# Performance work log

Hardware: AMD Instinct MI355X
Metric: run time of the kernel (lower is better)

Reference implementation:

```python
import jax, jax.numpy as jnp
from jax import lax
import numpy as np

D_IN, D, H, W, POOL = 1280, 100, 20, 3, 9
K_SIG, X0 = 1.0, 0.0
EPS = 1e-5


def setup_inputs() -> dict:
    key = jax.random.key(0)
    ks = jax.random.split(key, 8)
    N1, N2 = 512, 512
    return {
        "x1": jax.random.normal(ks[0], (N1, D_IN), jnp.float32),
        "x2": jax.random.normal(ks[1], (N2, D_IN), jnp.float32),
        "W1": jax.random.normal(ks[2], (D, D_IN), jnp.float32) * 0.02,
        "b1": jnp.zeros((D,), jnp.float32),
        "W2": jax.random.normal(ks[3], (H, 2 * D), jnp.float32) * 0.05,
        "b2": jnp.zeros((H,), jnp.float32),
        "bn1_g": jnp.ones((H,), jnp.float32),
        "bn1_b": jnp.zeros((H,), jnp.float32),
        "conv_w": jax.random.normal(ks[4], (1, H, 2 * W + 1, 2 * W + 1), jnp.float32) * 0.05,
        "conv_b": jnp.zeros((1,), jnp.float32),
        "bn2_g": jnp.ones((1,), jnp.float32),
        "bn2_b": jnp.zeros((1,), jnp.float32),
        "gamma": jnp.zeros((1,), jnp.float32),
    }


def reference(x1, x2, W1, b1, W2, b2, bn1_g, bn1_b, conv_w, conv_b, bn2_g, bn2_b, gamma):
    N1, N2 = x1.shape[0], x2.shape[0]
    # fc1 projection (relu1/dropout1 are defined but unused in the original forward)
    a = (x1 @ W1.T + b1)[None]          # [1, N1, D]
    c = (x2 @ W1.T + b2 * 0 + b1)[None] if False else (x2 @ W1.T + b1)[None]  # [1, N2, D]
    # broadcast pairwise |diff| and product -> [1, N1, N2, 2D]
    diff = jnp.abs(a[:, :, None, :] - c[:, None, :, :])
    mul = a[:, :, None, :] * c[:, None, :, :]
    m = jnp.concatenate([diff, mul], axis=-1).reshape(-1, 2 * D)  # [N1*N2, 2D]
    # fc2
    m = m @ W2.T + b2                    # [N1*N2, H]
    # BatchNorm1d in training mode: batch statistics, biased variance
    mu = m.mean(axis=0)
    var = m.var(axis=0)
    m = (m - mu) * lax.rsqrt(var + EPS) * bn1_g + bn1_b
    m = jax.nn.relu(m)
    m = m.reshape(1, N1, N2, H).transpose(0, 3, 1, 2)  # NCHW [1, H, N1, N2]
    # 7x7 conv, padding=W
    C = lax.conv_general_dilated(m, conv_w, (1, 1), [(W, W), (W, W)])
    C = C + conv_b.reshape(1, -1, 1, 1)
    # BatchNorm2d (training mode, biased variance over N,H,W per channel)
    mu2 = C.mean(axis=(0, 2, 3), keepdims=True)
    var2 = C.var(axis=(0, 2, 3), keepdims=True)
    C = (C - mu2) * lax.rsqrt(var2 + EPS) * bn2_g.reshape(1, -1, 1, 1) + bn2_b.reshape(1, -1, 1, 1)
    C = jax.nn.sigmoid(C)
    # MaxPool2d(9, padding=4): stride = kernel, -inf padding
    p = POOL // 2
    B = lax.reduce_window(C, -jnp.inf, lax.max, (1, 1, POOL, POOL), (1, 1, POOL, POOL),
                          [(0, 0), (0, 0), (p, p), (p, p)])
    # mean / unbiased std over dims (1, 2) keepdim
    mean = B.mean(axis=(1, 2), keepdims=True)
    std = jnp.sqrt(B.var(axis=(1, 2), keepdims=True, ddof=1) + EPS)
    Q = jax.nn.relu(B - mean - gamma.reshape(()) * std)
    phat = Q.sum() / (jnp.sign(Q).sum() + 1.0)
    phat = jnp.clip(jax.nn.sigmoid(K_SIG * (phat - X0)), 0.0, 1.0)
    return phat, C
```

## Files before the change

kernel.cpp:

```cpp
#include <hip/hip_runtime.h>
#include <hip/hip_bf16.h>
#include <math.h>

#define N1 512
#define N2 512
#define DIN 1280
#define DD 100
#define HH 20
#define NPIX (N1*N2)
#define PB 57

typedef short bf16x8 __attribute__((ext_vector_type(8)));
typedef float f32x4 __attribute__((ext_vector_type(4)));

static constexpr size_t WS_PP    = 0;
static constexpr size_t WS_W1T   = 409600;
static constexpr size_t WS_W2B   = 537600;
static constexpr size_t WS_M     = 541696;
static constexpr size_t WS_CRAW  = WS_M + 5242880;
static constexpr size_t WS_STATS = WS_CRAW + 262144;
static constexpr size_t WS_B     = WS_STATS + 64;

__global__ __launch_bounds__(256) void kP(const float* __restrict__ W1,
                                          const float* __restrict__ W2,
                                          float* __restrict__ w1t,
                                          unsigned short* __restrict__ w2b,
                                          float* __restrict__ stats) {
  const int tid = threadIdx.x;
  if (blockIdx.x >= 160) {
    int idx = (blockIdx.x - 160) * 256 + tid;
    if (blockIdx.x == 160 && tid < 64) stats[tid] = 0.0f;
    if (idx < 224 * 32) {
      int k = idx >> 5, n = idx & 31;
      float v = (n < HH && k < 200) ? W2[n * 200 + k] : 0.0f;
      __hip_bfloat16 b = __float2bfloat16(v);
      w2b[idx] = *reinterpret_cast<unsigned short*>(&b);
    }
    return;
  }
  __shared__ float sT[32][33];
  const int bx = blockIdx.x % 40, by = blockIdx.x / 40;
  const int tx = tid & 31, ty = tid >> 5;
#pragma unroll
  for (int e = 0; e < 4; ++e) {
    int h = by * 32 + ty + e * 8, k = bx * 32 + tx;
    sT[ty + e * 8][tx] = (h < DD) ? W1[(size_t)h * DIN + k] : 0.0f;
  }
  __syncthreads();
#pragma unroll
  for (int e = 0; e < 4; ++e) {
    int k = bx * 32 + ty + e * 8, h = by * 32 + tx;
    if (h < DD) w1t[(size_t)k * DD + h] = sT[tx][ty + e * 8];
  }
}

__global__ __launch_bounds__(256) void kA(const float* __restrict__ x1,
                                          const float* __restrict__ x2,
                                          const float* __restrict__ w1t,
                                          float* __restrict__ pp) {
  const int tid = threadIdx.x;
  const int w  = __builtin_amdgcn_readfirstlane(tid >> 6);
  const int rp = w >> 1, hh = w & 1;
  const int h = hh * 64 + (tid & 63);
  if (h >= DD) return;
  const int kq = blockIdx.x & 3;
  const int r0 = (blockIdx.x >> 2) * 4 + rp * 2;
  const float* xb = (r0 < N1) ? (x1 + (size_t)r0 * DIN) : (x2 + (size_t)(r0 - N1) * DIN);
  const float* xr0 = xb + kq * 320;
  const float* xr1 = xb + DIN + kq * 320;
  const float* w1p = w1t + (size_t)kq * 320 * DD + h;
  float a00 = 0.f, a01 = 0.f, a10 = 0.f, a11 = 0.f;
#pragma unroll 8
  for (int k = 0; k < 320; k += 2) {
    float wA = w1p[(size_t)k * DD];
    float wB = w1p[(size_t)(k + 1) * DD];
    a00 = fmaf(wA, xr0[k], a00); a01 = fmaf(wB, xr0[k + 1], a01);
    a10 = fmaf(wA, xr1[k], a10); a11 = fmaf(wB, xr1[k + 1], a11);
  }
  pp[(size_t)kq * 102400 + (size_t)r0 * DD + h] = a00 + a01;
  pp[(size_t)kq * 102400 + (size_t)(r0 + 1) * DD + h] = a10 + a11;
}

__global__ __launch_bounds__(256, 2) void kB(const float* __restrict__ pp,
                                             const float* __restrict__ b1,
                                             const unsigned short* __restrict__ w2b,
                                             float* __restrict__ m,
                                             float* __restrict__ stats) {
  __shared__ float sA[8][132];
  __shared__ float sC[64][132];
  __shared__ float wred[4][40];
  const int tid = threadIdx.x;
  const int bi = blockIdx.x >> 3, bj = blockIdx.x & 7;
  for (int idx = tid; idx < 72 * 33; idx += 256) {
    int r = idx / 33, d4 = idx % 33;
    float4 v = {0.f, 0.f, 0.f, 0.f};
    if (d4 < 25) {
      size_t row = (r < 8) ? (size_t)(bi * 8 + r) : (size_t)(N1 + bj * 64 + (r - 8));
      const float* base = pp + row * DD;
      float4 a0 = ((const float4*)base)[d4];
      float4 a1 = ((const float4*)(base + 102400))[d4];
      float4 a2 = ((const float4*)(base + 204800))[d4];
      float4 a3 = ((const float4*)(base + 307200))[d4];
      float4 bb = ((const float4*)b1)[d4];
      v.x = a0.x + a1.x + a2.x + a3.x + bb.x;
      v.y = a0.y + a1.y + a2.y + a3.y + bb.y;
      v.z = a0.z + a1.z + a2.z + a3.z + bb.z;
      v.w = a0.w + a1.w + a2.w + a3.w + bb.w;
    }
    if (r < 8) *(float4*)&sA[r][4 * d4] = v;
    else       *(float4*)&sC[r - 8][4 * d4] = v;
  }
  __syncthreads();
  const int w = tid >> 6, lane = tid & 63;
  const int ln = lane & 15, q = lane >> 4;
  const int jj = w * 16 + ln;
  bf16x8 af[7][2];
#pragma unroll
  for (int ks = 0; ks < 7; ++ks)
#pragma unroll
    for (int t = 0; t < 2; ++t) {
      bf16x8 v;
#pragma unroll
      for (int e = 0; e < 8; ++e)
        v[e] = (short)w2b[(ks * 32 + q * 8 + e) * 32 + ln + 16 * t];
      af[ks][t] = v;
    }
  int dOf[14];
  bool isP[14];
  float4 cH[14];
#pragma unroll
  for (int hx = 0; hx < 14; ++hx) {
    int kk = (hx >> 1) * 32 + q * 8 + (hx & 1) * 4;
    isP[hx] = kk >= 100;
    dOf[hx] = isP[hx] ? kk - 100 : kk;
    cH[hx] = *(const float4*)&sC[jj][dOf[hx]];
  }
  float st_s[8], st_q[8];
#pragma unroll
  for (int r = 0; r < 8; ++r) { st_s[r] = 0.f; st_q[r] = 0.f; }
  const int gj = bj * 64 + jj;
#pragma unroll 1
  for (int ii = 0; ii < 8; ++ii) {
    bf16x8 bf[7];
#pragma unroll
    for (int ks = 0; ks < 7; ++ks) {
      float4 a0 = *(const float4*)&sA[ii][dOf[2 * ks]];
      float4 a1 = *(const float4*)&sA[ii][dOf[2 * ks + 1]];
      float4 c0 = cH[2 * ks], c1 = cH[2 * ks + 1];
      float f0 = isP[2*ks]   ? a0.x * c0.x : fabsf(a0.x - c0.x);
      float f1 = isP[2*ks]   ? a0.y * c0.y : fabsf(a0.y - c0.y);
      float f2 = isP[2*ks]   ? a0.z * c0.z : fabsf(a0.z - c0.z);
      float f3 = isP[2*ks]   ? a0.w * c0.w : fabsf(a0.w - c0.w);
      float f4 = isP[2*ks+1] ? a1.x * c1.x : fabsf(a1.x - c1.x);
      float f5 = isP[2*ks+1] ? a1.y * c1.y : fabsf(a1.y - c1.y);
      float f6 = isP[2*ks+1] ? a1.z * c1.z : fabsf(a1.z - c1.z);
      float f7 = isP[2*ks+1] ? a1.w * c1.w : fabsf(a1.w - c1.w);
      union { bf16x8 v; __hip_bfloat162 h2[4]; } u;
      u.h2[0] = __float22bfloat162_rn(make_float2(f0, f1));
      u.h2[1] = __float22bfloat162_rn(make_float2(f2, f3));
      u.h2[2] = __float22bfloat162_rn(make_float2(f4, f5));
      u.h2[3] = __float22bfloat162_rn(make_float2(f6, f7));
      bf[ks] = u.v;
    }
    f32x4 acc0 = {0.f, 0.f, 0.f, 0.f}, acc1 = {0.f, 0.f, 0.f, 0.f};
#pragma unroll
    for (int ks = 0; ks < 7; ++ks) {
      acc0 = __builtin_amdgcn_mfma_f32_16x16x32_bf16(af[ks][0], bf[ks], acc0, 0, 0, 0);
      acc1 = __builtin_amdgcn_mfma_f32_16x16x32_bf16(af[ks][1], bf[ks], acc1, 0, 0, 0);
    }
    const size_t pix = (size_t)(bi * 8 + ii) * N2 + gj;
#pragma unroll
    for (int r = 0; r < 4; ++r) {
      m[(size_t)(4 * q + r) * NPIX + pix] = acc0[r];
      st_s[r] += acc0[r];
      st_q[r] += acc0[r] * acc0[r];
    }
    if (q == 0) {
#pragma unroll
      for (int r = 0; r < 4; ++r)
        m[(size_t)(16 + r) * NPIX + pix] = acc1[r];
    }
#pragma unroll
    for (int r = 0; r < 4; ++r) {
      st_s[4 + r] += acc1[r];
      st_q[4 + r] += acc1[r] * acc1[r];
    }
  }
#pragma unroll
  for (int r = 0; r < 8; ++r) {
#pragma unroll
    for (int off = 1; off < 16; off <<= 1) {
      st_s[r] += __shfl_xor(st_s[r], off);
      st_q[r] += __shfl_xor(st_q[r], off);
    }
  }
  if (ln == 0) {
#pragma unroll
    for (int r = 0; r < 4; ++r) {
      wred[w][4 * q + r]      = st_s[r];
      wred[w][20 + 4 * q + r] = st_q[r];
    }
    if (q == 0) {
#pragma unroll
      for (int r = 0; r < 4; ++r) {
        wred[w][16 + r] = st_s[4 + r];
        wred[w][36 + r] = st_q[4 + r];
      }
    }
  }
  __syncthreads();
  if (tid < 40)
    atomicAdd(&stats[tid], wred[0][tid] + wred[1][tid] + wred[2][tid] + wred[3][tid]);
}

__global__ __launch_bounds__(256, 2) void kD(const float* __restrict__ m,
                                             const float* __restrict__ bn1g,
                                             const float* __restrict__ bn1b,
                                             const float* __restrict__ cw,
                                             float* __restrict__ stats,
                                             float* __restrict__ Craw) {
  __shared__ float sIn[2][4][22][40];
  __shared__ float sSc[HH], sSh[HH];
  __shared__ float wsum[4][2];
  const int tid = threadIdx.x;
  if (tid < HH) {
    float s = stats[tid], q = stats[HH + tid];
    float mu = s * (1.0f / NPIX);
    float var = q * (1.0f / NPIX) - mu * mu;
    float g = bn1g[tid] / sqrtf(var + 1e-5f);
    sSc[tid] = g;
    sSh[tid] = bn1b[tid] - mu * g;
  }
  const int by = (blockIdx.x >> 4) * 16, bx = (blockIdx.x & 15) * 32;
  const int w = tid >> 6, lane = tid & 63;
  const int gxs = bx + lane - 4;
  const bool colOk = (lane < 40) && (gxs >= 0) && (gxs < N2);
  float ld[22];
  {
    const float* mp = m + (size_t)w * NPIX + gxs;
#pragma unroll
    for (int r = 0; r < 22; ++r) {
      int gy = by + r - 3;
      ld[r] = (colOk && gy >= 0 && gy < N1) ? mp[(size_t)gy * N2] : 0.0f;
    }
  }
  __syncthreads();
  if (lane < 40) {
    float sc = sSc[w], sh = sSh[w];
#pragma unroll
    for (int r = 0; r < 22; ++r) {
      int gy = by + r - 3;
      bool ok = colOk && gy >= 0 && gy < N1;
      sIn[0][w][r][lane] = ok ? fmaxf(fmaf(ld[r], sc, sh), 0.0f) : 0.0f;
    }
  }
  __syncthreads();
  const int ty = tid >> 4, tx = tid & 15;
  float acc00 = 0.f, acc01 = 0.f;
#pragma unroll 1
  for (int cc = 0; cc < 5; ++cc) {
    if (cc < 4) {
      const float* mp = m + (size_t)((cc + 1) * 4 + w) * NPIX + gxs;
#pragma unroll
      for (int r = 0; r < 22; ++r) {
        int gy = by + r - 3;
        ld[r] = (colOk && gy >= 0 && gy < N1) ? mp[(size_t)gy * N2] : 0.0f;
      }
    }
    const int cur = cc & 1;
#pragma unroll 1
    for (int ch4 = 0; ch4 < 4; ++ch4) {
      float2 win[7][5];
#pragma unroll
      for (int rr = 0; rr < 7; ++rr)
#pragma unroll
        for (int qq = 0; qq < 5; ++qq)
          win[rr][qq] = *(const float2*)&sIn[cur][ch4][ty + rr][2 * tx + 2 * qq];
      const float* wch = cw + (cc * 4 + ch4) * 49;
#pragma unroll
      for (int ky = 0; ky < 7; ++ky)
#pragma unroll
        for (int kx = 0; kx < 7; ++kx) {
          float wt = wch[ky * 7 + kx];
          float e0 = ((kx + 1) & 1) ? win[ky][(kx + 1) >> 1].y : win[ky][(kx + 1) >> 1].x;
          float e1 = ((kx + 2) & 1) ? win[ky][(kx + 2) >> 1].y : win[ky][(kx + 2) >> 1].x;
          acc00 = fmaf(e0, wt, acc00);
          acc01 = fmaf(e1, wt, acc01);
        }
    }
    __syncthreads();
    if (cc < 4 && lane < 40) {
      int ch = (cc + 1) * 4 + w;
      float sc = sSc[ch], sh = sSh[ch];
#pragma unroll
      for (int r = 0; r < 22; ++r) {
        int gy = by + r - 3;
        bool ok = colOk && gy >= 0 && gy < N1;
        sIn[cur ^ 1][w][r][lane] = ok ? fmaxf(fmaf(ld[r], sc, sh), 0.0f) : 0.0f;
      }
    }
    __syncthreads();
  }
  const int oy = by + ty, ox = bx + 2 * tx;
  float2 r0 = {acc00, acc01};
  *(float2*)&Craw[(size_t)oy * N2 + ox] = r0;
  float s = acc00 + acc01;
  float q = acc00 * acc00 + acc01 * acc01;
#pragma unroll
  for (int off = 32; off; off >>= 1) {
    s += __shfl_xor(s, off);
    q += __shfl_xor(q, off);
  }
  if (lane == 0) { wsum[w][0] = s; wsum[w][1] = q; }
  __syncthreads();
  if (tid < 2) {
    float v = wsum[0][tid] + wsum[1][tid] + wsum[2][tid] + wsum[3][tid];
    atomicAdd(&stats[2 * HH + tid], v);
  }
}

__global__ __launch_bounds__(256) void kE2M(const float* __restrict__ Craw,
                                            const float* __restrict__ stats,
                                            const float* __restrict__ bn2g,
                                            const float* __restrict__ bn2b,
                                            float* __restrict__ Cout,
                                            float* __restrict__ B) {
  const int w = blockIdx.x * 4 + (threadIdx.x >> 6);
  const int lane = threadIdx.x & 63;
  float s = stats[2 * HH], q = stats[2 * HH + 1];
  float mu = s * (1.0f / NPIX);
  float var = q * (1.0f / NPIX) - mu * mu;
  float g = bn2g[0] / sqrtf(var + 1e-5f);
  float b = bn2b[0] - mu * g;
  if (w >= PB * PB) return;
  const int wy = w / PB, wx = w % PB;
  const int y0 = wy * 9 - 4, x0 = wx * 9 - 4;
  float mx = -1e30f;
  for (int e = lane; e < 144; e += 64) {
    int dy = e / 12, dx = e % 12;
    int y = y0 + dy, x = x0 + dx;
    bool inWin = (dy < 9) && (dx < 9);
    bool claim = (y >= 0) && (y < N1) && (x >= 0) && (x < N2) &&
                 (dy < 9 || wy == PB - 1) && (dx < 9 || wx == PB - 1);
    if (claim) {
      float z = Craw[(size_t)y * N2 + x] * g + b;
      float sg = 1.0f / (1.0f + expf(-z));
      Cout[(size_t)y * N2 + x] = sg;
      if (inWin) mx = fmaxf(mx, sg);
    }
  }
#pragma unroll
  for (int off = 32; off; off >>= 1) mx = fmaxf(mx, __shfl_xor(mx, off));
  if (lane == 0) B[w] = mx;
}

__global__ __launch_bounds__(1024) void kF(const float* __restrict__ B,
                                           const float* __restrict__ gamma,
                                           float* __restrict__ out0) {
  __shared__ float sB[PB * PB];
  __shared__ float cm[PB], cs[PB];
  __shared__ float r1[16], r2[16];
  const int tid = threadIdx.x;
  for (int i = tid; i < PB * PB; i += 1024) sB[i] = B[i];
  __syncthreads();
  if (tid < PB * 16) {
    int c = tid >> 4, g = tid & 15;
    float s = 0.0f;
    for (int h = g; h < PB; h += 16) s += sB[h * PB + c];
#pragma unroll
    for (int off = 1; off < 16; off <<= 1) s += __shfl_xor(s, off);
    float mean = s / (float)PB;
    float v = 0.0f;
    for (int h = g; h < PB; h += 16) { float d = sB[h * PB + c] - mean; v += d * d; }
#pragma unroll
    for (int off = 1; off < 16; off <<= 1) v += __shfl_xor(v, off);
    if (g == 0) {
      cm[c] = mean;
      cs[c] = sqrtf(v / (float)(PB - 1) + 1e-5f);
    }
  }
  __syncthreads();
  const float g = gamma[0];
  float sq = 0.0f, cnt = 0.0f;
  for (int i = tid; i < PB * PB; i += 1024) {
    int w = i % PB;
    float qv = sB[i] - cm[w] - g * cs[w];
    if (qv > 0.0f) { sq += qv; cnt += 1.0f; }
  }
#pragma unroll
  for (int off = 32; off; off >>= 1) {
    sq += __shfl_xor(sq, off);
    cnt += __shfl_xor(cnt, off);
  }
  if ((tid & 63) == 0) { r1[tid >> 6] = sq; r2[tid >> 6] = cnt; }
  __syncthreads();
  if (tid == 0) {
    float S = 0.f, Cn = 0.f;
#pragma unroll
    for (int e = 0; e < 16; ++e) { S += r1[e]; Cn += r2[e]; }
    float phat = S / (Cn + 1.0f);
    float sig = 1.0f / (1.0f + expf(-phat));
    out0[0] = fminf(fmaxf(sig, 0.0f), 1.0f);
  }
}

extern "C" void kernel_launch(void* const* d_in, const int* in_sizes, int n_in,
                              void* d_out, int out_size, void* d_ws, size_t ws_size,
                              hipStream_t stream) {
  const float* x1    = (const float*)d_in[0];
  const float* x2    = (const float*)d_in[1];
  const float* W1    = (const float*)d_in[2];
  const float* b1    = (const float*)d_in[3];
  const float* W2    = (const float*)d_in[4];
  const float* bn1g  = (const float*)d_in[6];
  const float* bn1b  = (const float*)d_in[7];
  const float* convw = (const float*)d_in[8];
  const float* bn2g  = (const float*)d_in[10];
  const float* bn2b  = (const float*)d_in[11];
  const float* gamma = (const float*)d_in[12];

  float* ws    = (float*)d_ws;
  float* pp    = ws + WS_PP;
  float* w1t   = ws + WS_W1T;
  unsigned short* w2b = (unsigned short*)(ws + WS_W2B);
  float* m     = ws + WS_M;
  float* Craw  = ws + WS_CRAW;
  float* stats = ws + WS_STATS;
  float* Bp    = ws + WS_B;
  float* out   = (float*)d_out;

  kP<<<188, 256, 0, stream>>>(W1, W2, w1t, w2b, stats);
  kA<<<1024, 256, 0, stream>>>(x1, x2, w1t, pp);
  kB<<<512, 256, 0, stream>>>(pp, b1, w2b, m, stats);
  kD<<<512, 256, 0, stream>>>(m, bn1g, bn1b, convw, stats, Craw);
  kE2M<<<(PB * PB + 3) / 4, 256, 0, stream>>>(Craw, stats, bn2g, bn2b, out + 1, Bp);
  kF<<<1, 1024, 0, stream>>>(Bp, gamma, out);
}
```

Before: 92.17 us.

## Split conv over channel groups with register-blocked rows and separate reduction kernel

The 7x7 conv kernel is reworked so that each block handles one group of 4 input channels (grid y = 5) over a 32x32 tile. Each thread computes 4 output rows x 2 columns, which reuses every loaded shared-memory row across several outputs. Partial results for the 5 channel groups are written to a new workspace buffer. A new kernel kE1 then sums the partials, writes Craw and accumulates the BN2 statistics. The goal is more parallelism and less redundant LDS traffic, at the cost of an extra 5x NPIX partial write and read plus one more kernel launch.

```diff
diff --git a/kernel.cpp b/kernel.cpp
--- a/kernel.cpp
+++ b/kernel.cpp
@@ -17,7 +17,8 @@
 static constexpr size_t WS_W1T   = 409600;
 static constexpr size_t WS_W2B   = 537600;
 static constexpr size_t WS_M     = 541696;
-static constexpr size_t WS_CRAW  = WS_M + 5242880;
+static constexpr size_t WS_PART  = WS_M + 5242880;
+static constexpr size_t WS_CRAW  = WS_PART + 1310720;
 static constexpr size_t WS_STATS = WS_CRAW + 262144;
 static constexpr size_t WS_B     = WS_STATS + 64;
 
@@ -213,109 +214,100 @@
     atomicAdd(&stats[tid], wred[0][tid] + wred[1][tid] + wred[2][tid] + wred[3][tid]);
 }
 
-__global__ __launch_bounds__(256, 2) void kD(const float* __restrict__ m,
+__global__ __launch_bounds__(128, 2) void kD(const float* __restrict__ m,
                                              const float* __restrict__ bn1g,
                                              const float* __restrict__ bn1b,
                                              const float* __restrict__ cw,
-                                             float* __restrict__ stats,
-                                             float* __restrict__ Craw) {
-  __shared__ float sIn[2][4][22][40];
-  __shared__ float sSc[HH], sSh[HH];
-  __shared__ float wsum[4][2];
+                                             const float* __restrict__ stats,
+                                             float* __restrict__ part) {
+  __shared__ float sIn[4][38][42];
+  __shared__ float sSc[4], sSh[4];
   const int tid = threadIdx.x;
-  if (tid < HH) {
-    float s = stats[tid], q = stats[HH + tid];
+  const int cs = blockIdx.y;
+  if (tid < 4) {
+    int ch = cs * 4 + tid;
+    float s = stats[ch], q = stats[HH + ch];
     float mu = s * (1.0f / NPIX);
     float var = q * (1.0f / NPIX) - mu * mu;
-    float g = bn1g[tid] / sqrtf(var + 1e-5f);
+    float g = bn1g[ch] / sqrtf(var + 1e-5f);
     sSc[tid] = g;
-    sSh[tid] = bn1b[tid] - mu * g;
-  }
-  const int by = (blockIdx.x >> 4) * 16, bx = (blockIdx.x & 15) * 32;
-  const int w = tid >> 6, lane = tid & 63;
-  const int gxs = bx + lane - 4;
-  const bool colOk = (lane < 40) && (gxs >= 0) && (gxs < N2);
-  float ld[22];
-  {
-    const float* mp = m + (size_t)w * NPIX + gxs;
-#pragma unroll
-    for (int r = 0; r < 22; ++r) {
-      int gy = by + r - 3;
-      ld[r] = (colOk && gy >= 0 && gy < N1) ? mp[(size_t)gy * N2] : 0.0f;
-    }
-  }
-  __syncthreads();
-  if (lane < 40) {
-    float sc = sSc[w], sh = sSh[w];
-#pragma unroll
-    for (int r = 0; r < 22; ++r) {
-      int gy = by + r - 3;
-      bool ok = colOk && gy >= 0 && gy < N1;
-      sIn[0][w][r][lane] = ok ? fmaxf(fmaf(ld[r], sc, sh), 0.0f) : 0.0f;
-    }
+    sSh[tid] = bn1b[ch] - mu * g;
+  }
+  __syncthreads();
+  const int by = (blockIdx.x >> 4) * 32, bx = (blockIdx.x & 15) * 32;
+  for (int idx = tid; idx < 4 * 38 * 20; idx += 128) {
+    int ch4 = idx / 760, rem = idx % 760;
+    int r = rem / 20, c2 = rem % 20;
+    int gy = by + r - 3, gx = bx + 2 * c2 - 4;
+    float2 v = {0.f, 0.f};
+    if (gy >= 0 && gy < N1 && gx >= 0 && gx < N2) {
+      const float* mp = m + (size_t)(cs * 4 + ch4) * NPIX;
+      float2 raw = *(const float2*)&mp[(size_t)gy * N2 + gx];
+      float sc = sSc[ch4], sh = sSh[ch4];
+      v.x = fmaxf(fmaf(raw.x, sc, sh), 0.0f);
+      v.y = fmaxf(fmaf(raw.y, sc, sh), 0.0f);
+    }
+    *(float2*)&sIn[ch4][r][2 * c2] = v;
   }
   __syncthreads();
   const int ty = tid >> 4, tx = tid & 15;
-  float acc00 = 0.f, acc01 = 0.f;
+  float acc[4][2];
+#pragma unroll
+  for (int o = 0; o < 4; ++o) { acc[o][0] = 0.f; acc[o][1] = 0.f; }
 #pragma unroll 1
-  for (int cc = 0; cc < 5; ++cc) {
-    if (cc < 4) {
-      const float* mp = m + (size_t)((cc + 1) * 4 + w) * NPIX + gxs;
-#pragma unroll
-      for (int r = 0; r < 22; ++r) {
-        int gy = by + r - 3;
-        ld[r] = (colOk && gy >= 0 && gy < N1) ? mp[(size_t)gy * N2] : 0.0f;
-      }
-    }
-    const int cur = cc & 1;
-#pragma unroll 1
-    for (int ch4 = 0; ch4 < 4; ++ch4) {
-      float2 win[7][5];
-#pragma unroll
-      for (int rr = 0; rr < 7; ++rr)
-#pragma unroll
-        for (int qq = 0; qq < 5; ++qq)
-          win[rr][qq] = *(const float2*)&sIn[cur][ch4][ty + rr][2 * tx + 2 * qq];
-      const float* wch = cw + (cc * 4 + ch4) * 49;
-#pragma unroll
-      for (int ky = 0; ky < 7; ++ky)
+  for (int ch4 = 0; ch4 < 4; ++ch4) {
+    const float* wch = cw + (cs * 4 + ch4) * 49;
+#pragma unroll
+    for (int wr = 0; wr < 10; ++wr) {
+      float2 row[5];
+#pragma unroll
+      for (int qq = 0; qq < 5; ++qq)
+        row[qq] = *(const float2*)&sIn[ch4][4 * ty + wr][2 * tx + 2 * qq];
+#pragma unroll
+      for (int o = 0; o < 4; ++o) {
+        if (o > wr || wr - o > 6) continue;
+        const int ky = wr - o;
 #pragma unroll
         for (int kx = 0; kx < 7; ++kx) {
           float wt = wch[ky * 7 + kx];
-          float e0 = ((kx + 1) & 1) ? win[ky][(kx + 1) >> 1].y : win[ky][(kx + 1) >> 1].x;
-          float e1 = ((kx + 2) & 1) ? win[ky][(kx + 2) >> 1].y : win[ky][(kx + 2) >> 1].x;
-          acc00 = fmaf(e0, wt, acc00);
-          acc01 = fmaf(e1, wt, acc01);
+          const int j0 = kx + 1, j1 = kx + 2;
+          float e0 = (j0 & 1) ? row[j0 >> 1].y : row[j0 >> 1].x;
+          float e1 = (j1 & 1) ? row[j1 >> 1].y : row[j1 >> 1].x;
+          acc[o][0] = fmaf(e0, wt, acc[o][0]);
+          acc[o][1] = fmaf(e1, wt, acc[o][1]);
         }
-    }
-    __syncthreads();
-    if (cc < 4 && lane < 40) {
-      int ch = (cc + 1) * 4 + w;
-      float sc = sSc[ch], sh = sSh[ch];
-#pragma unroll
-      for (int r = 0; r < 22; ++r) {
-        int gy = by + r - 3;
-        bool ok = colOk && gy >= 0 && gy < N1;
-        sIn[cur ^ 1][w][r][lane] = ok ? fmaxf(fmaf(ld[r], sc, sh), 0.0f) : 0.0f;
       }
     }
-    __syncthreads();
-  }
-  const int oy = by + ty, ox = bx + 2 * tx;
-  float2 r0 = {acc00, acc01};
-  *(float2*)&Craw[(size_t)oy * N2 + ox] = r0;
-  float s = acc00 + acc01;
-  float q = acc00 * acc00 + acc01 * acc01;
+  }
+  float* dst = part + (size_t)cs * NPIX;
+  const int ox = bx + 2 * tx;
+#pragma unroll
+  for (int o = 0; o < 4; ++o) {
+    const int oy = by + 4 * ty + o;
+    float2 r0 = {acc[o][0], acc[o][1]};
+    *(float2*)&dst[(size_t)oy * N2 + ox] = r0;
+  }
+}
+
+__global__ __launch_bounds__(256) void kE1(const float* __restrict__ part,
+                                           float* __restrict__ stats,
+                                           float* __restrict__ Craw) {
+  __shared__ float wred[4][2];
+  const int i = blockIdx.x * 256 + threadIdx.x;
+  float s5 = part[i] + part[NPIX + i] + part[2 * NPIX + i] + part[3 * NPIX + i] + part[4 * NPIX + i];
+  Craw[i] = s5;
+  float s = s5, q = s5 * s5;
+  const int lane = threadIdx.x & 63, wv = threadIdx.x >> 6;
 #pragma unroll
   for (int off = 32; off; off >>= 1) {
     s += __shfl_xor(s, off);
     q += __shfl_xor(q, off);
   }
-  if (lane == 0) { wsum[w][0] = s; wsum[w][1] = q; }
-  __syncthreads();
-  if (tid < 2) {
-    float v = wsum[0][tid] + wsum[1][tid] + wsum[2][tid] + wsum[3][tid];
-    atomicAdd(&stats[2 * HH + tid], v);
+  if (lane == 0) { wred[wv][0] = s; wred[wv][1] = q; }
+  __syncthreads();
+  if (threadIdx.x < 2) {
+    float v = wred[0][threadIdx.x] + wred[1][threadIdx.x] + wred[2][threadIdx.x] + wred[3][threadIdx.x];
+    atomicAdd(&stats[2 * HH + threadIdx.x], v);
   }
 }
 
@@ -424,6 +416,7 @@
   float* w1t   = ws + WS_W1T;
   unsigned short* w2b = (unsigned short*)(ws + WS_W2B);
   float* m     = ws + WS_M;
+  float* part  = ws + WS_PART;
   float* Craw  = ws + WS_CRAW;
   float* stats = ws + WS_STATS;
   float* Bp    = ws + WS_B;
@@ -432,7 +425,8 @@
   kP<<<188, 256, 0, stream>>>(W1, W2, w1t, w2b, stats);
   kA<<<1024, 256, 0, stream>>>(x1, x2, w1t, pp);
   kB<<<512, 256, 0, stream>>>(pp, b1, w2b, m, stats);
-  kD<<<512, 256, 0, stream>>>(m, bn1g, bn1b, convw, stats, Craw);
+  kD<<<dim3(256, 5), 128, 0, stream>>>(m, bn1g, bn1b, convw, stats, part);
+  kE1<<<1024, 256, 0, stream>>>(part, stats, Craw);
   kE2M<<<(PB * PB + 3) / 4, 256, 0, stream>>>(Craw, stats, bn2g, bn2b, out + 1, Bp);
   kF<<<1, 1024, 0, stream>>>(Bp, gamma, out);
 }
```

After: 95.30 us. 1.03x slower.

## Store fc2 activations as bf16 and fuse final reduction into pooling kernel

Applied to the files above, without the earlier changes.

The fc2 output tensor m, written by kB and read by kD, is now stored in bf16 instead of fp32. This halves the bytes in the largest intermediate round-trip through memory. The final phat kernel is folded into the sigmoid/maxpool kernel through a last-block-done atomic counter, which removes one launch, and the W2 conversion and stats zeroing move from kP into kA. The trade-offs are a loss of precision in the BN1 input and a counter that is zeroed by kA on each call, though kA's stats clearing only covers indices below 64, which includes index 60, so the counter does get reset.

```diff
diff --git a/kernel.cpp b/kernel.cpp
--- a/kernel.cpp
+++ b/kernel.cpp
@@ -9,27 +9,56 @@
 #define HH 20
 #define NPIX (N1*N2)
 #define PB 57
+#define NWIN (PB*PB)
+#define E2M_BLOCKS ((NWIN + 3) / 4)
 
 typedef short bf16x8 __attribute__((ext_vector_type(8)));
 typedef float f32x4 __attribute__((ext_vector_type(4)));
+
+static __device__ __forceinline__ float bf16f(unsigned short u) {
+  union { unsigned int i; float f; } c;
+  c.i = ((unsigned int)u) << 16;
+  return c.f;
+}
 
 static constexpr size_t WS_PP    = 0;
 static constexpr size_t WS_W1T   = 409600;
 static constexpr size_t WS_W2B   = 537600;
 static constexpr size_t WS_M     = 541696;
-static constexpr size_t WS_CRAW  = WS_M + 5242880;
+static constexpr size_t WS_CRAW  = WS_M + 2621440;
 static constexpr size_t WS_STATS = WS_CRAW + 262144;
 static constexpr size_t WS_B     = WS_STATS + 64;
 
 __global__ __launch_bounds__(256) void kP(const float* __restrict__ W1,
+                                          float* __restrict__ w1t) {
+  const int tid = threadIdx.x;
+  __shared__ float sT[32][33];
+  const int bx = blockIdx.x % 40, by = blockIdx.x / 40;
+  const int tx = tid & 31, ty = tid >> 5;
+#pragma unroll
+  for (int e = 0; e < 4; ++e) {
+    int h = by * 32 + ty + e * 8, k = bx * 32 + tx;
+    sT[ty + e * 8][tx] = (h < DD) ? W1[(size_t)h * DIN + k] : 0.0f;
+  }
+  __syncthreads();
+#pragma unroll
+  for (int e = 0; e < 4; ++e) {
+    int k = bx * 32 + ty + e * 8, h = by * 32 + tx;
+    if (h < DD) w1t[(size_t)k * DD + h] = sT[tx][ty + e * 8];
+  }
+}
+
+__global__ __launch_bounds__(256) void kA(const float* __restrict__ x1,
+                                          const float* __restrict__ x2,
+                                          const float* __restrict__ w1t,
                                           const float* __restrict__ W2,
-                                          float* __restrict__ w1t,
+                                          float* __restrict__ pp,
                                           unsigned short* __restrict__ w2b,
                                           float* __restrict__ stats) {
   const int tid = threadIdx.x;
-  if (blockIdx.x >= 160) {
-    int idx = (blockIdx.x - 160) * 256 + tid;
-    if (blockIdx.x == 160 && tid < 64) stats[tid] = 0.0f;
+  if (blockIdx.x >= 1024) {
+    int idx = (blockIdx.x - 1024) * 256 + tid;
+    if (blockIdx.x == 1024 && tid < 64) stats[tid] = 0.0f;
     if (idx < 224 * 32) {
       int k = idx >> 5, n = idx & 31;
       float v = (n < HH && k < 200) ? W2[n * 200 + k] : 0.0f;
@@ -38,27 +67,6 @@
     }
     return;
   }
-  __shared__ float sT[32][33];
-  const int bx = blockIdx.x % 40, by = blockIdx.x / 40;
-  const int tx = tid & 31, ty = tid >> 5;
-#pragma unroll
-  for (int e = 0; e < 4; ++e) {
-    int h = by * 32 + ty + e * 8, k = bx * 32 + tx;
-    sT[ty + e * 8][tx] = (h < DD) ? W1[(size_t)h * DIN + k] : 0.0f;
-  }
-  __syncthreads();
-#pragma unroll
-  for (int e = 0; e < 4; ++e) {
-    int k = bx * 32 + ty + e * 8, h = by * 32 + tx;
-    if (h < DD) w1t[(size_t)k * DD + h] = sT[tx][ty + e * 8];
-  }
-}
-
-__global__ __launch_bounds__(256) void kA(const float* __restrict__ x1,
-                                          const float* __restrict__ x2,
-                                          const float* __restrict__ w1t,
-                                          float* __restrict__ pp) {
-  const int tid = threadIdx.x;
   const int w  = __builtin_amdgcn_readfirstlane(tid >> 6);
   const int rp = w >> 1, hh = w & 1;
   const int h = hh * 64 + (tid & 63);
@@ -84,7 +92,7 @@
 __global__ __launch_bounds__(256, 2) void kB(const float* __restrict__ pp,
                                              const float* __restrict__ b1,
                                              const unsigned short* __restrict__ w2b,
-                                             float* __restrict__ m,
+                                             unsigned short* __restrict__ m16,
                                              float* __restrict__ stats) {
   __shared__ float sA[8][132];
   __shared__ float sC[64][132];
@@ -171,14 +179,17 @@
     const size_t pix = (size_t)(bi * 8 + ii) * N2 + gj;
 #pragma unroll
     for (int r = 0; r < 4; ++r) {
-      m[(size_t)(4 * q + r) * NPIX + pix] = acc0[r];
+      __hip_bfloat16 hb = __float2bfloat16(acc0[r]);
+      m16[(size_t)(4 * q + r) * NPIX + pix] = *reinterpret_cast<unsigned short*>(&hb);
       st_s[r] += acc0[r];
       st_q[r] += acc0[r] * acc0[r];
     }
     if (q == 0) {
 #pragma unroll
-      for (int r = 0; r < 4; ++r)
-        m[(size_t)(16 + r) * NPIX + pix] = acc1[r];
+      for (int r = 0; r < 4; ++r) {
+        __hip_bfloat16 hb = __float2bfloat16(acc1[r]);
+        m16[(size_t)(16 + r) * NPIX + pix] = *reinterpret_cast<unsigned short*>(&hb);
+      }
     }
 #pragma unroll
     for (int r = 0; r < 4; ++r) {
@@ -213,7 +224,7 @@
     atomicAdd(&stats[tid], wred[0][tid] + wred[1][tid] + wred[2][tid] + wred[3][tid]);
 }
 
-__global__ __launch_bounds__(256, 2) void kD(const float* __restrict__ m,
+__global__ __launch_bounds__(256, 2) void kD(const unsigned short* __restrict__ m16,
                                              const float* __restrict__ bn1g,
                                              const float* __restrict__ bn1b,
                                              const float* __restrict__ cw,
@@ -235,13 +246,13 @@
   const int w = tid >> 6, lane = tid & 63;
   const int gxs = bx + lane - 4;
   const bool colOk = (lane < 40) && (gxs >= 0) && (gxs < N2);
-  float ld[22];
+  unsigned short ld[22];
   {
-    const float* mp = m + (size_t)w * NPIX + gxs;
+    const unsigned short* mp = m16 + (size_t)w * NPIX + gxs;
 #pragma unroll
     for (int r = 0; r < 22; ++r) {
       int gy = by + r - 3;
-      ld[r] = (colOk && gy >= 0 && gy < N1) ? mp[(size_t)gy * N2] : 0.0f;
+      ld[r] = (colOk && gy >= 0 && gy < N1) ? mp[(size_t)gy * N2] : 0;
     }
   }
   __syncthreads();
@@ -251,7 +262,7 @@
     for (int r = 0; r < 22; ++r) {
       int gy = by + r - 3;
       bool ok = colOk && gy >= 0 && gy < N1;
-      sIn[0][w][r][lane] = ok ? fmaxf(fmaf(ld[r], sc, sh), 0.0f) : 0.0f;
+      sIn[0][w][r][lane] = ok ? fmaxf(fmaf(bf16f(ld[r]), sc, sh), 0.0f) : 0.0f;
     }
   }
   __syncthreads();
@@ -260,11 +271,11 @@
 #pragma unroll 1
   for (int cc = 0; cc < 5; ++cc) {
     if (cc < 4) {
-      const float* mp = m + (size_t)((cc + 1) * 4 + w) * NPIX + gxs;
+      const unsigned short* mp = m16 + (size_t)((cc + 1) * 4 + w) * NPIX + gxs;
 #pragma unroll
       for (int r = 0; r < 22; ++r) {
         int gy = by + r - 3;
-        ld[r] = (colOk && gy >= 0 && gy < N1) ? mp[(size_t)gy * N2] : 0.0f;
+        ld[r] = (colOk && gy >= 0 && gy < N1) ? mp[(size_t)gy * N2] : 0;
       }
     }
     const int cur = cc & 1;
@@ -296,7 +307,7 @@
       for (int r = 0; r < 22; ++r) {
         int gy = by + r - 3;
         bool ok = colOk && gy >= 0 && gy < N1;
-        sIn[cur ^ 1][w][r][lane] = ok ? fmaxf(fmaf(ld[r], sc, sh), 0.0f) : 0.0f;
+        sIn[cur ^ 1][w][r][lane] = ok ? fmaxf(fmaf(bf16f(ld[r]), sc, sh), 0.0f) : 0.0f;
       }
     }
     __syncthreads();
@@ -319,85 +330,88 @@
   }
 }
 
-__global__ __launch_bounds__(256) void kE2M(const float* __restrict__ Craw,
-                                            const float* __restrict__ stats,
-                                            const float* __restrict__ bn2g,
-                                            const float* __restrict__ bn2b,
-                                            float* __restrict__ Cout,
-                                            float* __restrict__ B) {
-  const int w = blockIdx.x * 4 + (threadIdx.x >> 6);
-  const int lane = threadIdx.x & 63;
-  float s = stats[2 * HH], q = stats[2 * HH + 1];
-  float mu = s * (1.0f / NPIX);
-  float var = q * (1.0f / NPIX) - mu * mu;
-  float g = bn2g[0] / sqrtf(var + 1e-5f);
-  float b = bn2b[0] - mu * g;
-  if (w >= PB * PB) return;
-  const int wy = w / PB, wx = w % PB;
-  const int y0 = wy * 9 - 4, x0 = wx * 9 - 4;
-  float mx = -1e30f;
-  for (int e = lane; e < 144; e += 64) {
-    int dy = e / 12, dx = e % 12;
-    int y = y0 + dy, x = x0 + dx;
-    bool inWin = (dy < 9) && (dx < 9);
-    bool claim = (y >= 0) && (y < N1) && (x >= 0) && (x < N2) &&
-                 (dy < 9 || wy == PB - 1) && (dx < 9 || wx == PB - 1);
-    if (claim) {
-      float z = Craw[(size_t)y * N2 + x] * g + b;
-      float sg = 1.0f / (1.0f + expf(-z));
-      Cout[(size_t)y * N2 + x] = sg;
-      if (inWin) mx = fmaxf(mx, sg);
-    }
-  }
-#pragma unroll
-  for (int off = 32; off; off >>= 1) mx = fmaxf(mx, __shfl_xor(mx, off));
-  if (lane == 0) B[w] = mx;
-}
-
-__global__ __launch_bounds__(1024) void kF(const float* __restrict__ B,
-                                           const float* __restrict__ gamma,
-                                           float* __restrict__ out0) {
-  __shared__ float sB[PB * PB];
+__global__ __launch_bounds__(256) void kE2MF(const float* __restrict__ Craw,
+                                             const float* __restrict__ stats,
+                                             const float* __restrict__ bn2g,
+                                             const float* __restrict__ bn2b,
+                                             const float* __restrict__ gamma,
+                                             float* __restrict__ Cout,
+                                             float* __restrict__ B,
+                                             int* __restrict__ cnt,
+                                             float* __restrict__ out0) {
+  __shared__ float sB[NWIN];
   __shared__ float cm[PB], cs[PB];
-  __shared__ float r1[16], r2[16];
+  __shared__ float r1[4], r2[4];
+  __shared__ int isLast;
   const int tid = threadIdx.x;
-  for (int i = tid; i < PB * PB; i += 1024) sB[i] = B[i];
-  __syncthreads();
-  if (tid < PB * 16) {
-    int c = tid >> 4, g = tid & 15;
+  const int wv = tid >> 6, lane = tid & 63;
+  const int w = blockIdx.x * 4 + wv;
+  {
+    float s = stats[2 * HH], q = stats[2 * HH + 1];
+    float mu = s * (1.0f / NPIX);
+    float var = q * (1.0f / NPIX) - mu * mu;
+    float g = bn2g[0] / sqrtf(var + 1e-5f);
+    float b = bn2b[0] - mu * g;
+    if (w < NWIN) {
+      const int wy = w / PB, wx = w % PB;
+      const int y0 = wy * 9 - 4, x0 = wx * 9 - 4;
+      float mx = -1e30f;
+      for (int e = lane; e < 144; e += 64) {
+        int dy = e / 12, dx = e % 12;
+        int y = y0 + dy, x = x0 + dx;
+        bool inWin = (dy < 9) && (dx < 9);
+        bool claim = (y >= 0) && (y < N1) && (x >= 0) && (x < N2) &&
+                     (dy < 9 || wy == PB - 1) && (dx < 9 || wx == PB - 1);
+        if (claim) {
+          float z = Craw[(size_t)y * N2 + x] * g + b;
+          float sg = 1.0f / (1.0f + expf(-z));
+          Cout[(size_t)y * N2 + x] = sg;
+          if (inWin) mx = fmaxf(mx, sg);
+        }
+      }
+#pragma unroll
+      for (int off = 32; off; off >>= 1) mx = fmaxf(mx, __shfl_xor(mx, off));
+      if (lane == 0) B[w] = mx;
+    }
+  }
+  __threadfence();
+  __syncthreads();
+  if (tid == 0) {
+    int old = atomicAdd(cnt, 1);
+    isLast = (old == E2M_BLOCKS - 1) ? 1 : 0;
+  }
+  __syncthreads();
+  if (!isLast) return;
+  __threadfence();
+  for (int i = tid; i < NWIN; i += 256) sB[i] = B[i];
+  __syncthreads();
+  if (tid < PB) {
     float s = 0.0f;
-    for (int h = g; h < PB; h += 16) s += sB[h * PB + c];
-#pragma unroll
-    for (int off = 1; off < 16; off <<= 1) s += __shfl_xor(s, off);
+    for (int h = 0; h < PB; ++h) s += sB[h * PB + tid];
     float mean = s / (float)PB;
     float v = 0.0f;
-    for (int h = g; h < PB; h += 16) { float d = sB[h * PB + c] - mean; v += d * d; }
-#pragma unroll
-    for (int off = 1; off < 16; off <<= 1) v += __shfl_xor(v, off);
-    if (g == 0) {
-      cm[c] = mean;
-      cs[c] = sqrtf(v / (float)(PB - 1) + 1e-5f);
-    }
+    for (int h = 0; h < PB; ++h) { float d = sB[h * PB + tid] - mean; v += d * d; }
+    cm[tid] = mean;
+    cs[tid] = sqrtf(v / (float)(PB - 1) + 1e-5f);
   }
   __syncthreads();
   const float g = gamma[0];
-  float sq = 0.0f, cnt = 0.0f;
-  for (int i = tid; i < PB * PB; i += 1024) {
-    int w = i % PB;
-    float qv = sB[i] - cm[w] - g * cs[w];
-    if (qv > 0.0f) { sq += qv; cnt += 1.0f; }
+  float sq = 0.0f, cnt2 = 0.0f;
+  for (int i = tid; i < NWIN; i += 256) {
+    int c = i % PB;
+    float qv = sB[i] - cm[c] - g * cs[c];
+    if (qv > 0.0f) { sq += qv; cnt2 += 1.0f; }
   }
 #pragma unroll
   for (int off = 32; off; off >>= 1) {
     sq += __shfl_xor(sq, off);
-    cnt += __shfl_xor(cnt, off);
-  }
-  if ((tid & 63) == 0) { r1[tid >> 6] = sq; r2[tid >> 6] = cnt; }
+    cnt2 += __shfl_xor(cnt2, off);
+  }
+  if (lane == 0) { r1[wv] = sq; r2[wv] = cnt2; }
   __syncthreads();
   if (tid == 0) {
-    float S = 0.f, Cn = 0.f;
-#pragma unroll
-    for (int e = 0; e < 16; ++e) { S += r1[e]; Cn += r2[e]; }
+    float S = r1[0] + r1[1] + r1[2] + r1[3];
+    float Cn = r2[0] + r2[1] + r2[2] + r2[3];
     float phat = S / (Cn + 1.0f);
     float sig = 1.0f / (1.0f + expf(-phat));
     out0[0] = fminf(fmaxf(sig, 0.0f), 1.0f);
@@ -423,16 +437,17 @@
   float* pp    = ws + WS_PP;
   float* w1t   = ws + WS_W1T;
   unsigned short* w2b = (unsigned short*)(ws + WS_W2B);
-  float* m     = ws + WS_M;
+  unsigned short* m16 = (unsigned short*)(ws + WS_M);
   float* Craw  = ws + WS_CRAW;
   float* stats = ws + WS_STATS;
+  int*   cnt   = (int*)(stats + 60);
   float* Bp    = ws + WS_B;
   float* out   = (float*)d_out;
 
-  kP<<<188, 256, 0, stream>>>(W1, W2, w1t, w2b, stats);
-  kA<<<1024, 256, 0, stream>>>(x1, x2, w1t, pp);
-  kB<<<512, 256, 0, stream>>>(pp, b1, w2b, m, stats);
-  kD<<<512, 256, 0, stream>>>(m, bn1g, bn1b, convw, stats, Craw);
-  kE2M<<<(PB * PB + 3) / 4, 256, 0, stream>>>(Craw, stats, bn2g, bn2b, out + 1, Bp);
-  kF<<<1, 1024, 0, stream>>>(Bp, gamma, out);
-}
+  kP<<<160, 256, 0, stream>>>(W1, w1t);
+  kA<<<1052, 256, 0, stream>>>(x1, x2, w1t, W2, pp, w2b, stats);
+  kB<<<512, 256, 0, stream>>>(pp, b1, w2b, m16, stats);
+  kD<<<512, 256, 0, stream>>>(m16, bn1g, bn1b, convw, stats, Craw);
+  kE2MF<<<E2M_BLOCKS, 256, 0, stream>>>(Craw, stats, bn2g, bn2b, gamma,
+                                        out + 1, Bp, cnt, out);
+}
```

After: 143.3 us. +55.4%, slower.
